# Kernel optimization log

Hardware: AMD Instinct MI355X
Metric: run time of the kernel (lower is better)

The kernel has to match this reference:

```python
import jax, jax.numpy as jnp
import numpy as np

D_MODEL = 1024
NUM_EXP = 64
EPS = 1e-9
B, L = 16, 2048


def setup_inputs() -> dict:
    key = jax.random.key(0)
    ks = jax.random.split(key, 12)
    s = 1.0 / np.sqrt(D_MODEL)
    inp = {
        "x": jax.random.normal(ks[0], (B, L, D_MODEL), dtype=jnp.float32),
        "n_indexes": jax.random.randint(ks[1], (B, NUM_EXP), 0, NUM_EXP),
        "mask": jax.random.randint(ks[2], (B, 1, L), 0, 2).astype(jnp.int32),
        "q_emb": jax.random.normal(ks[3], (NUM_EXP, D_MODEL), dtype=jnp.float32),
        "b_emb": jax.random.normal(ks[4], (NUM_EXP, D_MODEL), dtype=jnp.float32),
        "Wk": jax.random.normal(ks[5], (D_MODEL, D_MODEL), dtype=jnp.float32) * s,
        "bk": jnp.zeros((D_MODEL,), jnp.float32),
        "Wa": jax.random.normal(ks[6], (D_MODEL, D_MODEL), dtype=jnp.float32) * s,
        "ba": jnp.zeros((D_MODEL,), jnp.float32),
        "Wb": jax.random.normal(ks[7], (D_MODEL, D_MODEL), dtype=jnp.float32) * s,
        "bb": jnp.zeros((D_MODEL,), jnp.float32),
        "Ws": jax.random.normal(ks[8], (D_MODEL, D_MODEL), dtype=jnp.float32) * s,
        "bs": jnp.zeros((D_MODEL,), jnp.float32),
    }
    return inp


def reference(x, n_indexes, mask, q_emb, b_emb, Wk, bk, Wa, ba, Wb, bb, Ws, bs):
    # Dropout layers act as identity (eval mode).
    query_exp = q_emb[n_indexes]          # [B, E, D]
    bias_exp = b_emb[n_indexes]           # [B, E, D]
    x_key = x @ Wk.T + bk                 # [B, L, D]
    z = jnp.einsum('bed,bld->bel', query_exp, x_key) / np.sqrt(D_MODEL)  # [B, E, L]

    maskf = (mask != 0).astype(z.dtype)   # broadcast [B,1,L]
    class_a_fw = jax.nn.relu(z) * maskf
    class_b_fw = jax.nn.relu(-z) * maskf
    class_a_fw = class_a_fw / (class_a_fw.sum(-1, keepdims=True) + EPS)
    class_b_fw = class_b_fw / (class_b_fw.sum(-1, keepdims=True) + EPS)

    class_a = jnp.einsum('bel,bld->bed', class_a_fw, x @ Wa.T + ba) + bias_exp
    class_b = jnp.einsum('bel,bld->bed', class_b_fw, x @ Wb.T + bb) + bias_exp

    zt = jnp.swapaxes(z, -2, -1)          # [B, L, E]  (unmasked, as in source)
    class_a_bw = jax.nn.relu(zt)
    class_b_bw = jax.nn.relu(-zt)
    class_a_bw = class_a_bw / (class_a_bw.sum(-1, keepdims=True) + EPS)
    class_b_bw = class_b_bw / (class_b_bw.sum(-1, keepdims=True) + EPS)

    class_a = jnp.einsum('ble,bed->bld', class_a_bw, class_a)  # [B, L, D]
    class_b = jnp.einsum('ble,bed->bld', class_b_bw, class_b)

    selector = jax.nn.sigmoid(x @ Ws.T + bs)
    return selector * class_a + (1.0 - selector) * class_b
```

## Files before the change

### kernel.cpp

```cpp
#include <hip/hip_runtime.h>
#include <math.h>

#define D_MODEL 1024
#define NUM_EXP 64
#define B_SZ 16
#define L_SZ 2048

using bf16x8  = __attribute__((ext_vector_type(8))) __bf16;
using floatx4 = __attribute__((ext_vector_type(4))) float;
using ushort8 = __attribute__((ext_vector_type(8))) unsigned short;
using ushort4v = __attribute__((ext_vector_type(4))) unsigned short;

__device__ __forceinline__ unsigned short f2bf(float f) {
    union { float f; unsigned u; } x; x.f = f;
    unsigned r = (x.u + 0x7fffu + ((x.u >> 16) & 1u)) >> 16;
    return (unsigned short)r;
}
__device__ __forceinline__ float bf2f(unsigned short h) {
    union { unsigned u; float f; } x; x.u = ((unsigned)h) << 16;
    return x.f;
}

#define GLD16(gp, lp) __builtin_amdgcn_global_load_lds( \
    (const __attribute__((address_space(1))) unsigned int*)(gp), \
    (__attribute__((address_space(3))) unsigned int*)(lp), 16, 0, 0)

__global__ void k_convx(const float* __restrict__ in, unsigned short* __restrict__ outN,
                        unsigned short* __restrict__ outT)
{
    __shared__ unsigned short T[64][65];
    const int b = blockIdx.z;
    const int l0 = blockIdx.y * 64, c0 = blockIdx.x * 64;
    const int t = threadIdx.x;
    const int tr = t >> 4, tc = (t & 15) * 4;
    const float* src = in + ((long)b * L_SZ + l0) * D_MODEL + c0;
    unsigned short* dN = outN + ((long)b * L_SZ + l0) * D_MODEL + c0;
    #pragma unroll
    for (int i = 0; i < 4; i++) {
        int r = tr + i * 16;
        float4 v = *(const float4*)(src + (long)r * D_MODEL + tc);
        ushort4v u; u[0]=f2bf(v.x); u[1]=f2bf(v.y); u[2]=f2bf(v.z); u[3]=f2bf(v.w);
        *(ushort4v*)(dN + (long)r * D_MODEL + tc) = u;
        T[r][tc+0]=u[0]; T[r][tc+1]=u[1]; T[r][tc+2]=u[2]; T[r][tc+3]=u[3];
    }
    __syncthreads();
    unsigned short* dT = outT + ((long)b * D_MODEL + c0) * L_SZ + l0;
    #pragma unroll
    for (int i = 0; i < 4; i++) {
        int c = tr + i * 16;
        ushort4v u;
        u[0]=T[tc+0][c]; u[1]=T[tc+1][c]; u[2]=T[tc+2][c]; u[3]=T[tc+3][c];
        *(ushort4v*)(dT + (long)c * L_SZ + tc) = u;
    }
}

__global__ void k_transw(const float* __restrict__ in, unsigned short* __restrict__ outT)
{
    __shared__ unsigned short T[64][65];
    const int r0 = blockIdx.y * 64, c0 = blockIdx.x * 64;
    const int t = threadIdx.x;
    const int tr = t >> 4, tc = (t & 15) * 4;
    const float* src = in + (long)r0 * D_MODEL + c0;
    #pragma unroll
    for (int i = 0; i < 4; i++) {
        int r = tr + i * 16;
        float4 v = *(const float4*)(src + (long)r * D_MODEL + tc);
        T[r][tc+0]=f2bf(v.x); T[r][tc+1]=f2bf(v.y); T[r][tc+2]=f2bf(v.z); T[r][tc+3]=f2bf(v.w);
    }
    __syncthreads();
    unsigned short* dT = outT + ((long)c0) * D_MODEL + r0;
    #pragma unroll
    for (int i = 0; i < 4; i++) {
        int c = tr + i * 16;
        ushort4v u;
        u[0]=T[tc+0][c]; u[1]=T[tc+1][c]; u[2]=T[tc+2][c]; u[3]=T[tc+3][c];
        *(ushort4v*)(dT + (long)c * D_MODEL + tc) = u;
    }
}

__global__ void k_convert3(const float* __restrict__ a, const float* __restrict__ b,
                           const float* __restrict__ c,
                           unsigned short* __restrict__ oa, unsigned short* __restrict__ ob,
                           unsigned short* __restrict__ oc)
{
    long i = ((long)blockIdx.x * 256 + threadIdx.x) * 8;
    int which = (int)(i >> 20);
    long off = i & ((1L << 20) - 1);
    const float* src = which == 0 ? a : which == 1 ? b : c;
    unsigned short* dst = which == 0 ? oa : which == 1 ? ob : oc;
    float4 v0 = *(const float4*)(src + off);
    float4 v1 = *(const float4*)(src + off + 4);
    ushort8 r;
    r[0]=f2bf(v0.x); r[1]=f2bf(v0.y); r[2]=f2bf(v0.z); r[3]=f2bf(v0.w);
    r[4]=f2bf(v1.x); r[5]=f2bf(v1.y); r[6]=f2bf(v1.z); r[7]=f2bf(v1.w);
    *(ushort8*)(dst + off) = r;
}

__global__ void k_gather(const int* __restrict__ idx, const float* __restrict__ q_emb,
                         const float* __restrict__ b_emb, const float* __restrict__ bk,
                         unsigned short* __restrict__ qexp, float* __restrict__ bias_exp,
                         float* __restrict__ qbk)
{
    int be = blockIdx.x;
    int row = idx[be];
    int t = threadIdx.x;
    const float* qs = q_emb + (long)row * D_MODEL;
    const float* bsrc = b_emb + (long)row * D_MODEL;
    float4 q4 = *(const float4*)(qs + t * 4);
    float4 k4 = *(const float4*)(bk + t * 4);
    float4 b4 = *(const float4*)(bsrc + t * 4);
    ushort4v r; r[0]=f2bf(q4.x); r[1]=f2bf(q4.y); r[2]=f2bf(q4.z); r[3]=f2bf(q4.w);
    *(ushort4v*)(qexp + (long)be * D_MODEL + t * 4) = r;
    *(float4*)(bias_exp + (long)be * D_MODEL + t * 4) = b4;
    float p = q4.x*k4.x + q4.y*k4.y + q4.z*k4.z + q4.w*k4.w;
    #pragma unroll
    for (int o = 32; o > 0; o >>= 1) p += __shfl_down(p, o);
    __shared__ float red[4];
    if ((t & 63) == 0) red[t >> 6] = p;
    __syncthreads();
    if (t == 0) qbk[be] = red[0] + red[1] + red[2] + red[3];
}

__launch_bounds__(256)
__global__ void k_gemm_bt(const unsigned short* __restrict__ A,
                          const unsigned short* __restrict__ Bm,
                          const float* __restrict__ rowbias,
                          void* __restrict__ Cout,
                          int M, int N, int K, float scale, int flags,
                          long sA, long sB, long sC)
{
    __shared__ __align__(16) unsigned short As[64 * 32];
    __shared__ __align__(16) unsigned short Bs[64 * 32];
    const int bz = blockIdx.z;
    const unsigned short* Ab = A + (long)bz * sA;
    const unsigned short* Bb = Bm + (long)bz * sB;
    const int tid = threadIdx.x;
    const int wave = tid >> 6, lane = tid & 63;
    const int m0 = blockIdx.y * 64, n0 = blockIdx.x * 64;
    const int lrow = tid >> 2, lk = (tid & 3) * 8;
    const int q = lane >> 4, mr = lane & 15;

    floatx4 acc[4];
    floatx4 z4 = {0.f, 0.f, 0.f, 0.f};
    #pragma unroll
    for (int j = 0; j < 4; j++) acc[j] = z4;

    const unsigned short* Aptr = Ab + (long)(m0 + lrow) * K + lk;
    const unsigned short* Bptr = Bb + (long)(n0 + lrow) * K + lk;

    for (int k0 = 0; k0 < K; k0 += 32) {
        __syncthreads();
        *(ushort8*)&As[lrow * 32 + lk] = *(const ushort8*)(Aptr + k0);
        *(ushort8*)&Bs[lrow * 32 + lk] = *(const ushort8*)(Bptr + k0);
        __syncthreads();
        bf16x8 af = *(const bf16x8*)&As[(wave * 16 + mr) * 32 + q * 8];
        #pragma unroll
        for (int j = 0; j < 4; j++) {
            bf16x8 bfr = *(const bf16x8*)&Bs[(j * 16 + mr) * 32 + q * 8];
            acc[j] = __builtin_amdgcn_mfma_f32_16x16x32_bf16(af, bfr, acc[j], 0, 0, 0);
        }
    }
    #pragma unroll
    for (int j = 0; j < 4; j++) {
        int gn = n0 + j * 16 + mr;
        #pragma unroll
        for (int r = 0; r < 4; r++) {
            int gm = m0 + wave * 16 + q * 4 + r;
            float v = acc[j][r];
            if (rowbias) v += rowbias[(long)bz * M + gm];
            v *= scale;
            long cidx = (long)bz * sC + (long)gm * N + gn;
            if (flags & 1) ((unsigned short*)Cout)[cidx] = f2bf(v);
            else           ((float*)Cout)[cidx] = v;
        }
    }
}

__launch_bounds__(256)
__global__ void k_gemm_fw2(const unsigned short* __restrict__ A1,
                           const unsigned short* __restrict__ A2,
                           const unsigned short* __restrict__ Bt,
                           unsigned short* __restrict__ C1,
                           unsigned short* __restrict__ C2)
{
    __shared__ __align__(16) unsigned short As1[64 * 32];
    __shared__ __align__(16) unsigned short As2[64 * 32];
    __shared__ __align__(16) unsigned short Bs[64 * 32];
    const int bz = blockIdx.z;
    const int n0 = blockIdx.x * 64;
    const int tid = threadIdx.x;
    const int wave = tid >> 6, lane = tid & 63;
    const int lrow = tid >> 2, lk = (tid & 3) * 8;
    const int q = lane >> 4, mr = lane & 15;

    const unsigned short* a1p = A1 + ((long)bz * NUM_EXP + lrow) * L_SZ + lk;
    const unsigned short* a2p = A2 + ((long)bz * NUM_EXP + lrow) * L_SZ + lk;
    const unsigned short* bp  = Bt + ((long)bz * D_MODEL + n0 + lrow) * L_SZ + lk;

    floatx4 acc1[4], acc2[4];
    floatx4 z4 = {0.f, 0.f, 0.f, 0.f};
    #pragma unroll
    for (int j = 0; j < 4; j++) { acc1[j] = z4; acc2[j] = z4; }

    for (int k0 = 0; k0 < L_SZ; k0 += 32) {
        __syncthreads();
        *(ushort8*)&As1[lrow * 32 + lk] = *(const ushort8*)(a1p + k0);
        *(ushort8*)&As2[lrow * 32 + lk] = *(const ushort8*)(a2p + k0);
        *(ushort8*)&Bs[lrow * 32 + lk]  = *(const ushort8*)(bp + k0);
        __syncthreads();
        bf16x8 f1 = *(const bf16x8*)&As1[(wave * 16 + mr) * 32 + q * 8];
        bf16x8 f2 = *(const bf16x8*)&As2[(wave * 16 + mr) * 32 + q * 8];
        #pragma unroll
        for (int j = 0; j < 4; j++) {
            bf16x8 bb = *(const bf16x8*)&Bs[(j * 16 + mr) * 32 + q * 8];
            acc1[j] = __builtin_amdgcn_mfma_f32_16x16x32_bf16(f1, bb, acc1[j], 0, 0, 0);
            acc2[j] = __builtin_amdgcn_mfma_f32_16x16x32_bf16(f2, bb, acc2[j], 0, 0, 0);
        }
    }
    #pragma unroll
    for (int j = 0; j < 4; j++) {
        int gn = n0 + j * 16 + mr;
        #pragma unroll
        for (int r = 0; r < 4; r++) {
            int gm = wave * 16 + q * 4 + r;
            long cidx = ((long)bz * NUM_EXP + gm) * D_MODEL + gn;
            C1[cidx] = f2bf(acc1[j][r]);
            C2[cidx] = f2bf(acc2[j][r]);
        }
    }
}

__launch_bounds__(256)
__global__ void k_gemm_cls(const unsigned short* __restrict__ fwxA, const unsigned short* __restrict__ fwxB,
                           const unsigned short* __restrict__ Wa_, const unsigned short* __restrict__ Wb_,
                           const float* __restrict__ ba_, const float* __restrict__ bb_,
                           const float* __restrict__ wsA, const float* __restrict__ wsB,
                           const float* __restrict__ biasE,
                           unsigned short* __restrict__ aHi, unsigned short* __restrict__ aLo,
                           unsigned short* __restrict__ bHi, unsigned short* __restrict__ bLo)
{
    __shared__ __align__(16) unsigned short As[64 * 32];
    __shared__ __align__(16) unsigned short Bs[64 * 32];
    const int zz = blockIdx.z;
    const int side = zz >> 4, bz = zz & 15;
    const unsigned short* Ab = (side ? fwxB : fwxA) + (long)bz * NUM_EXP * D_MODEL;
    const unsigned short* Bb = side ? Wb_ : Wa_;
    const float* cb = side ? bb_ : ba_;
    const float* rw = (side ? wsB : wsA) + bz * NUM_EXP;
    const float* bE = biasE + (long)bz * NUM_EXP * D_MODEL;
    unsigned short* oHi = (side ? bHi : aHi) + (long)bz * NUM_EXP * D_MODEL;
    unsigned short* oLo = (side ? bLo : aLo) + (long)bz * NUM_EXP * D_MODEL;

    const int tid = threadIdx.x;
    const int wave = tid >> 6, lane = tid & 63;
    const int n0 = blockIdx.x * 64;
    const int lrow = tid >> 2, lk = (tid & 3) * 8;
    const int q = lane >> 4, mr = lane & 15;

    floatx4 acc[4];
    floatx4 z4 = {0.f, 0.f, 0.f, 0.f};
    #pragma unroll
    for (int j = 0; j < 4; j++) acc[j] = z4;

    const unsigned short* Aptr = Ab + (long)lrow * D_MODEL + lk;
    const unsigned short* Bptr = Bb + (long)(n0 + lrow) * D_MODEL + lk;

    for (int k0 = 0; k0 < D_MODEL; k0 += 32) {
        __syncthreads();
        *(ushort8*)&As[lrow * 32 + lk] = *(const ushort8*)(Aptr + k0);
        *(ushort8*)&Bs[lrow * 32 + lk] = *(const ushort8*)(Bptr + k0);
        __syncthreads();
        bf16x8 af = *(const bf16x8*)&As[(wave * 16 + mr) * 32 + q * 8];
        #pragma unroll
        for (int j = 0; j < 4; j++) {
            bf16x8 bfr = *(const bf16x8*)&Bs[(j * 16 + mr) * 32 + q * 8];
            acc[j] = __builtin_amdgcn_mfma_f32_16x16x32_bf16(af, bfr, acc[j], 0, 0, 0);
        }
    }
    #pragma unroll
    for (int j = 0; j < 4; j++) {
        int gn = n0 + j * 16 + mr;
        float cbv = cb[gn];
        #pragma unroll
        for (int r = 0; r < 4; r++) {
            int gm = wave * 16 + q * 4 + r;
            float v = acc[j][r] + rw[gm] * cbv + bE[(long)gm * D_MODEL + gn];
            unsigned short hi = f2bf(v);
            long tix = (long)gn * NUM_EXP + gm;
            oHi[tix] = hi;
            oLo[tix] = f2bf(v - bf2f(hi));
        }
    }
}

__launch_bounds__(256)
__global__ void k_gemm_sel(const unsigned short* __restrict__ A,
                           const unsigned short* __restrict__ Bm,
                           const float* __restrict__ bias,
                           unsigned short* __restrict__ C)
{
    __shared__ __align__(16) unsigned short As[128 * 32];
    __shared__ __align__(16) unsigned short Bs[128 * 32];
    const int tid = threadIdx.x;
    const int wave = tid >> 6, lane = tid & 63;
    const int q = lane >> 4, mr = lane & 15;
    const int wm = wave & 1, wn = wave >> 1;
    const int blk = blockIdx.x;
    const int m0 = ((blk & 7) * 32 + (blk >> 6)) * 128;
    const int n0 = ((blk >> 3) & 7) * 128;

    int rows[2], kofs8[2];
    #pragma unroll
    for (int c = 0; c < 2; c++) {
        int s = c * 256 + tid;
        int row = s >> 2;
        rows[c] = row;
        kofs8[c] = ((s & 3) ^ ((row >> 1) & 3)) * 8;
    }
    const unsigned short* gA0 = A + (long)(m0 + rows[0]) * 1024 + kofs8[0];
    const unsigned short* gA1 = A + (long)(m0 + rows[1]) * 1024 + kofs8[1];
    const unsigned short* gB0 = Bm + (long)(n0 + rows[0]) * 1024 + kofs8[0];
    const unsigned short* gB1 = Bm + (long)(n0 + rows[1]) * 1024 + kofs8[1];
    unsigned short* LA0 = &As[(0 * 256 + wave * 64) * 8];
    unsigned short* LA1 = &As[(1 * 256 + wave * 64) * 8];
    unsigned short* LB0 = &Bs[(0 * 256 + wave * 64) * 8];
    unsigned short* LB1 = &Bs[(1 * 256 + wave * 64) * 8];

    floatx4 acc[4][4];
    floatx4 z4 = {0.f, 0.f, 0.f, 0.f};
    #pragma unroll
    for (int i = 0; i < 4; i++)
        #pragma unroll
        for (int j = 0; j < 4; j++) acc[i][j] = z4;

    const int kread = (q ^ ((mr >> 1) & 3)) * 8;

    for (int k0 = 0; k0 < 1024; k0 += 32) {
        __syncthreads();
        GLD16(gA0 + k0, LA0);
        GLD16(gA1 + k0, LA1);
        GLD16(gB0 + k0, LB0);
        GLD16(gB1 + k0, LB1);
        __syncthreads();
        bf16x8 af[4], bfv[4];
        #pragma unroll
        for (int i = 0; i < 4; i++)
            af[i] = *(const bf16x8*)&As[(wm * 64 + i * 16 + mr) * 32 + kread];
        #pragma unroll
        for (int j = 0; j < 4; j++)
            bfv[j] = *(const bf16x8*)&Bs[(wn * 64 + j * 16 + mr) * 32 + kread];
        #pragma unroll
        for (int i = 0; i < 4; i++)
            #pragma unroll
            for (int j = 0; j < 4; j++)
                acc[i][j] = __builtin_amdgcn_mfma_f32_16x16x32_bf16(af[i], bfv[j], acc[i][j], 0, 0, 0);
    }

    #pragma unroll
    for (int i = 0; i < 4; i++) {
        #pragma unroll
        for (int j = 0; j < 4; j++) {
            int gn = n0 + wn * 64 + j * 16 + mr;
            float cbv = bias[gn];
            #pragma unroll
            for (int r = 0; r < 4; r++) {
                int gm = m0 + wm * 64 + i * 16 + q * 4 + r;
                C[(long)gm * 1024 + gn] = f2bf(acc[i][j][r] + cbv);
            }
        }
    }
}

__global__ void k_fwnorm(const float* __restrict__ z, const int* __restrict__ mask,
                         unsigned short* __restrict__ a_fw, unsigned short* __restrict__ b_fw,
                         float* __restrict__ wsum_a, float* __restrict__ wsum_b)
{
    int be = blockIdx.x;
    int b = be >> 6;
    const float* zr = z + (long)be * L_SZ;
    const int* mr = mask + (long)b * L_SZ;
    int tid = threadIdx.x;
    float sa = 0.f, sb = 0.f;
    for (int l = tid; l < L_SZ; l += 256) {
        float v = zr[l];
        if (mr[l] != 0) { sa += fmaxf(v, 0.f); sb += fmaxf(-v, 0.f); }
    }
    #pragma unroll
    for (int o = 32; o > 0; o >>= 1) { sa += __shfl_down(sa, o); sb += __shfl_down(sb, o); }
    __shared__ float red[8];
    int wave = tid >> 6, lane = tid & 63;
    if (lane == 0) { red[wave] = sa; red[4 + wave] = sb; }
    __syncthreads();
    float ta = red[0] + red[1] + red[2] + red[3];
    float tb = red[4] + red[5] + red[6] + red[7];
    float ia = 1.f / (ta + 1e-9f), ib = 1.f / (tb + 1e-9f);
    if (tid == 0) { wsum_a[be] = ta * ia; wsum_b[be] = tb * ib; }
    for (int l = tid; l < L_SZ; l += 256) {
        float v = zr[l];
        float m = (mr[l] != 0) ? 1.f : 0.f;
        a_fw[(long)be * L_SZ + l] = f2bf(fmaxf(v, 0.f) * m * ia);
        b_fw[(long)be * L_SZ + l] = f2bf(fmaxf(-v, 0.f) * m * ib);
    }
}

__global__ void k_bwnorm(const float* __restrict__ z, unsigned short* __restrict__ a_bw,
                         unsigned short* __restrict__ b_bw)
{
    int r = blockIdx.x * 256 + threadIdx.x;
    int b = r >> 11, l = r & 2047;
    const float* zb = z + (long)b * NUM_EXP * L_SZ + l;
    float sa = 0.f, sb = 0.f;
    float va[NUM_EXP];
    #pragma unroll 8
    for (int e = 0; e < NUM_EXP; e++) {
        float v = zb[(long)e * L_SZ];
        va[e] = v;
        sa += fmaxf(v, 0.f); sb += fmaxf(-v, 0.f);
    }
    float ia = 1.f / (sa + 1e-9f), ib = 1.f / (sb + 1e-9f);
    unsigned short* ar = a_bw + (long)r * NUM_EXP;
    unsigned short* br = b_bw + (long)r * NUM_EXP;
    #pragma unroll 8
    for (int e = 0; e < NUM_EXP; e++) {
        float v = va[e];
        ar[e] = f2bf(fmaxf(v, 0.f) * ia);
        br[e] = f2bf(fmaxf(-v, 0.f) * ib);
    }
}

__launch_bounds__(256)
__global__ void k_final_mfma(const unsigned short* __restrict__ aw,
                             const unsigned short* __restrict__ bw,
                             const unsigned short* __restrict__ caHi,
                             const unsigned short* __restrict__ caLo,
                             const unsigned short* __restrict__ cbHi,
                             const unsigned short* __restrict__ cbLo,
                             const unsigned short* __restrict__ selbf,
                             float* __restrict__ out)
{
    __shared__ __align__(16) unsigned short Aa[64 * 72];
    __shared__ __align__(16) unsigned short Ab[64 * 72];
    __shared__ __align__(16) unsigned short BaH[64 * 72];
    __shared__ __align__(16) unsigned short BaL[64 * 72];
    __shared__ __align__(16) unsigned short BbH[64 * 72];
    __shared__ __align__(16) unsigned short BbL[64 * 72];
    const int bz = blockIdx.z;
    const int l0 = blockIdx.y * 64, d0 = blockIdx.x * 64;
    const int tid = threadIdx.x;
    const int wave = tid >> 6, lane = tid & 63;
    const int q = lane >> 4, mr = lane & 15;

    const unsigned short* awb = aw + ((long)bz * L_SZ + l0) * NUM_EXP;
    const unsigned short* bwb = bw + ((long)bz * L_SZ + l0) * NUM_EXP;
    const long cbase = ((long)bz * D_MODEL + d0) * NUM_EXP;

    #pragma unroll
    for (int c = 0; c < 2; c++) {
        int idx = c * 256 + tid;
        int row = idx >> 3, kc = (idx & 7) * 8;
        int lw = row * 72 + kc;
        long ga = (long)row * NUM_EXP + kc;
        *(ushort8*)&Aa[lw]  = *(const ushort8*)(awb + ga);
        *(ushort8*)&Ab[lw]  = *(const ushort8*)(bwb + ga);
        *(ushort8*)&BaH[lw] = *(const ushort8*)(caHi + cbase + ga);
        *(ushort8*)&BaL[lw] = *(const ushort8*)(caLo + cbase + ga);
        *(ushort8*)&BbH[lw] = *(const ushort8*)(cbHi + cbase + ga);
        *(ushort8*)&BbL[lw] = *(const ushort8*)(cbLo + cbase + ga);
    }
    __syncthreads();

    floatx4 accA[4], accB[4];
    floatx4 z4 = {0.f, 0.f, 0.f, 0.f};
    #pragma unroll
    for (int j = 0; j < 4; j++) { accA[j] = z4; accB[j] = z4; }

    #pragma unroll
    for (int ks = 0; ks < 2; ks++) {
        int ko = ks * 32 + q * 8;
        bf16x8 fa = *(const bf16x8*)&Aa[(wave * 16 + mr) * 72 + ko];
        bf16x8 fb = *(const bf16x8*)&Ab[(wave * 16 + mr) * 72 + ko];
        #pragma unroll
        for (int j = 0; j < 4; j++) {
            int bo = (j * 16 + mr) * 72 + ko;
            accA[j] = __builtin_amdgcn_mfma_f32_16x16x32_bf16(fa, *(const bf16x8*)&BaH[bo], accA[j], 0, 0, 0);
            accA[j] = __builtin_amdgcn_mfma_f32_16x16x32_bf16(fa, *(const bf16x8*)&BaL[bo], accA[j], 0, 0, 0);
            accB[j] = __builtin_amdgcn_mfma_f32_16x16x32_bf16(fb, *(const bf16x8*)&BbH[bo], accB[j], 0, 0, 0);
            accB[j] = __builtin_amdgcn_mfma_f32_16x16x32_bf16(fb, *(const bf16x8*)&BbL[bo], accB[j], 0, 0, 0);
        }
    }

    #pragma unroll
    for (int j = 0; j < 4; j++) {
        #pragma unroll
        for (int r = 0; r < 4; r++) {
            int gl = l0 + wave * 16 + q * 4 + r;
            int gd = d0 + j * 16 + mr;
            long o = ((long)bz * L_SZ + gl) * D_MODEL + gd;
            float s = 1.f / (1.f + __expf(-bf2f(selbf[o])));
            out[o] = s * accA[j][r] + (1.f - s) * accB[j][r];
        }
    }
}

extern "C" void kernel_launch(void* const* d_in, const int* in_sizes, int n_in,
                              void* d_out, int out_size, void* d_ws, size_t ws_size,
                              hipStream_t stream)
{
    const float* x     = (const float*)d_in[0];
    const int*   nidx  = (const int*)d_in[1];
    const int*   mask  = (const int*)d_in[2];
    const float* q_emb = (const float*)d_in[3];
    const float* b_emb = (const float*)d_in[4];
    const float* Wk    = (const float*)d_in[5];
    const float* bk    = (const float*)d_in[6];
    const float* Wa    = (const float*)d_in[7];
    const float* ba    = (const float*)d_in[8];
    const float* Wb    = (const float*)d_in[9];
    const float* bb    = (const float*)d_in[10];
    const float* Ws    = (const float*)d_in[11];
    const float* bs    = (const float*)d_in[12];
    float* out = (float*)d_out;

    constexpr long BLD = (long)B_SZ * L_SZ * D_MODEL;
    constexpr long BEL = (long)B_SZ * NUM_EXP * L_SZ;
    constexpr long BED = (long)B_SZ * NUM_EXP * D_MODEL;
    constexpr long DD  = (long)D_MODEL * D_MODEL;

    char* w = (char*)d_ws;
    size_t off = 0;
    auto carve = [&](size_t bytes) { char* p = w + off; off += (bytes + 255) & ~(size_t)255; return p; };
    unsigned short* x_bf   = (unsigned short*)carve(BLD * 2);
    unsigned short* x_bfT  = (unsigned short*)carve(BLD * 2);
    unsigned short* wkT_bf = (unsigned short*)carve(DD * 2);
    unsigned short* wa_bf  = (unsigned short*)carve(DD * 2);
    unsigned short* wb_bf  = (unsigned short*)carve(DD * 2);
    unsigned short* ws_bf  = (unsigned short*)carve(DD * 2);
    unsigned short* qexp   = (unsigned short*)carve(BED * 2);
    float*          bias_e = (float*)carve(BED * 4);
    float*          qbk    = (float*)carve(B_SZ * NUM_EXP * 4);
    unsigned short* qk     = (unsigned short*)carve(BED * 2);
    float*          z      = (float*)carve(BEL * 4);
    unsigned short* a_fw   = (unsigned short*)carve(BEL * 2);
    unsigned short* b_fw   = (unsigned short*)carve(BEL * 2);
    float*          wsum_a = (float*)carve(B_SZ * NUM_EXP * 4);
    float*          wsum_b = (float*)carve(B_SZ * NUM_EXP * 4);
    unsigned short* a_bw   = (unsigned short*)carve(BEL * 2);
    unsigned short* b_bw   = (unsigned short*)carve(BEL * 2);
    unsigned short* fwx_a  = (unsigned short*)carve(BED * 2);
    unsigned short* fwx_b  = (unsigned short*)carve(BED * 2);
    unsigned short* caHi   = (unsigned short*)carve(BED * 2);
    unsigned short* caLo   = (unsigned short*)carve(BED * 2);
    unsigned short* cbHi   = (unsigned short*)carve(BED * 2);
    unsigned short* cbLo   = (unsigned short*)carve(BED * 2);
    if (ws_size < off) return;
    unsigned short* selbf = x_bfT;

    k_convx<<<dim3(16, 32, B_SZ), 256, 0, stream>>>(x, x_bf, x_bfT);
    k_transw<<<dim3(16, 16), 256, 0, stream>>>(Wk, wkT_bf);
    k_convert3<<<(3 * DD) / 2048, 256, 0, stream>>>(Wa, Wb, Ws, wa_bf, wb_bf, ws_bf);
    k_gather<<<B_SZ * NUM_EXP, 256, 0, stream>>>(nidx, q_emb, b_emb, bk, qexp, bias_e, qbk);

    k_gemm_bt<<<dim3(16, 1, B_SZ), 256, 0, stream>>>(qexp, wkT_bf, nullptr, qk,
        NUM_EXP, D_MODEL, D_MODEL, 1.f, 1, (long)NUM_EXP * D_MODEL, 0, (long)NUM_EXP * D_MODEL);

    k_gemm_bt<<<dim3(32, 1, B_SZ), 256, 0, stream>>>(qk, x_bf, qbk, z,
        NUM_EXP, L_SZ, D_MODEL, 1.f / 32.f, 0,
        (long)NUM_EXP * D_MODEL, (long)L_SZ * D_MODEL, (long)NUM_EXP * L_SZ);

    k_fwnorm<<<B_SZ * NUM_EXP, 256, 0, stream>>>(z, mask, a_fw, b_fw, wsum_a, wsum_b);
    k_bwnorm<<<(B_SZ * L_SZ) / 256, 256, 0, stream>>>(z, a_bw, b_bw);

    k_gemm_fw2<<<dim3(16, 1, B_SZ), 256, 0, stream>>>(a_fw, b_fw, x_bfT, fwx_a, fwx_b);

    k_gemm_sel<<<2048, 256, 0, stream>>>(x_bf, ws_bf, bs, selbf);

    k_gemm_cls<<<dim3(16, 1, 32), 256, 0, stream>>>(fwx_a, fwx_b, wa_bf, wb_bf, ba, bb,
        wsum_a, wsum_b, bias_e, caHi, caLo, cbHi, cbLo);

    k_final_mfma<<<dim3(16, 32, B_SZ), 256, 0, stream>>>(a_bw, b_bw, caHi, caLo, cbHi, cbLo, selbf, out);
}
```

Measured before the change: 546.3 us.

## Rewrite selector GEMM with 256x256 tiles and multi-stage async LDS pipeline

The selector GEMM goes from 128x128 tiles with a synchronous load-then-compute loop to 256x256 tiles on 512-thread blocks. Global loads go straight to LDS with double buffering and stay several stages ahead of compute. The MFMA blocks are interleaved with barriers and priority hints. The aim is to hide memory latency behind MFMA work and raise data reuse per block. In exchange it uses more LDS and registers, and relies on hand-tuned vmcnt waits that must stay correct.

```diff
diff --git a/kernel.cpp b/kernel.cpp
--- a/kernel.cpp
+++ b/kernel.cpp
@@ -293,78 +293,101 @@
     }
 }
 
-__launch_bounds__(256)
+__launch_bounds__(512, 2)
 __global__ void k_gemm_sel(const unsigned short* __restrict__ A,
                            const unsigned short* __restrict__ Bm,
                            const float* __restrict__ bias,
                            unsigned short* __restrict__ C)
 {
-    __shared__ __align__(16) unsigned short As[128 * 32];
-    __shared__ __align__(16) unsigned short Bs[128 * 32];
+    __shared__ __align__(16) unsigned short As[2][2][8192];
+    __shared__ __align__(16) unsigned short Bs[2][2][8192];
+
     const int tid = threadIdx.x;
-    const int wave = tid >> 6, lane = tid & 63;
+    const int wid = tid >> 6, lane = tid & 63;
     const int q = lane >> 4, mr = lane & 15;
-    const int wm = wave & 1, wn = wave >> 1;
-    const int blk = blockIdx.x;
-    const int m0 = ((blk & 7) * 32 + (blk >> 6)) * 128;
-    const int n0 = ((blk >> 3) & 7) * 128;
-
-    int rows[2], kofs8[2];
-    #pragma unroll
-    for (int c = 0; c < 2; c++) {
-        int s = c * 256 + tid;
-        int row = s >> 2;
-        rows[c] = row;
-        kofs8[c] = ((s & 3) ^ ((row >> 1) & 3)) * 8;
-    }
-    const unsigned short* gA0 = A + (long)(m0 + rows[0]) * 1024 + kofs8[0];
-    const unsigned short* gA1 = A + (long)(m0 + rows[1]) * 1024 + kofs8[1];
-    const unsigned short* gB0 = Bm + (long)(n0 + rows[0]) * 1024 + kofs8[0];
-    const unsigned short* gB1 = Bm + (long)(n0 + rows[1]) * 1024 + kofs8[1];
-    unsigned short* LA0 = &As[(0 * 256 + wave * 64) * 8];
-    unsigned short* LA1 = &As[(1 * 256 + wave * 64) * 8];
-    unsigned short* LB0 = &Bs[(0 * 256 + wave * 64) * 8];
-    unsigned short* LB1 = &Bs[(1 * 256 + wave * 64) * 8];
-
-    floatx4 acc[4][4];
+    const int wm = wid >> 2, wn = wid & 3;
+    const int kread = (q ^ ((mr >> 1) & 3)) * 8;
+
+    const int bid = blockIdx.x;
+    const int wg = (bid & 7) * 64 + (bid >> 3);
+    const int m0 = (wg >> 2) * 256;
+    const int n0 = (wg & 3) * 256;
+
+    const unsigned short* Ag = A + (long)m0 * 1024;
+    const unsigned short* Bg = Bm + (long)n0 * 1024;
+
+    const int srow = tid >> 2;
+    const int sgrp = (tid & 3) ^ ((srow >> 1) & 3);
+    const long soff = (long)srow * 1024 + sgrp * 8;
+    const int ldst = wid * 64 * 8;
+
+    auto STAGE = [&](int g) {
+        int tile = g >> 2; if (tile > 15) tile = 15;
+        const int kh = (g >> 1) & 1, isB = g & 1;
+        const unsigned short* src = (isB ? Bg : Ag) + (long)tile * 64 + kh * 32 + soff;
+        unsigned short* dst = (isB ? &Bs[0][0][0] : &As[0][0][0])
+                              + ((tile & 1) * 2 + kh) * 8192 + ldst;
+        GLD16(src, dst);
+        GLD16(src + 128 * 1024, dst + 4096);
+    };
+
+    floatx4 acc[8][4];
     floatx4 z4 = {0.f, 0.f, 0.f, 0.f};
     #pragma unroll
-    for (int i = 0; i < 4; i++)
+    for (int i = 0; i < 8; i++)
         #pragma unroll
         for (int j = 0; j < 4; j++) acc[i][j] = z4;
 
-    const int kread = (q ^ ((mr >> 1) & 3)) * 8;
-
-    for (int k0 = 0; k0 < 1024; k0 += 32) {
-        __syncthreads();
-        GLD16(gA0 + k0, LA0);
-        GLD16(gA1 + k0, LA1);
-        GLD16(gB0 + k0, LB0);
-        GLD16(gB1 + k0, LB1);
-        __syncthreads();
-        bf16x8 af[4], bfv[4];
-        #pragma unroll
-        for (int i = 0; i < 4; i++)
-            af[i] = *(const bf16x8*)&As[(wm * 64 + i * 16 + mr) * 32 + kread];
-        #pragma unroll
-        for (int j = 0; j < 4; j++)
-            bfv[j] = *(const bf16x8*)&Bs[(wn * 64 + j * 16 + mr) * 32 + kread];
-        #pragma unroll
-        for (int i = 0; i < 4; i++)
+    STAGE(0); STAGE(1); STAGE(2); STAGE(3); STAGE(4); STAGE(5);
+    asm volatile("s_waitcnt vmcnt(4)" ::: "memory");
+    __builtin_amdgcn_s_barrier();
+
+    for (int t = 0; t < 16; t++) {
+        const unsigned short* Abuf = &As[t & 1][0][0];
+        const unsigned short* Bbuf = &Bs[t & 1][0][0];
+        bf16x8 bfr[4];
+        #pragma unroll
+        for (int p = 0; p < 4; p++) {
+            const int kh = p >> 1, mh = p & 1;
+            bf16x8 af[4];
             #pragma unroll
-            for (int j = 0; j < 4; j++)
-                acc[i][j] = __builtin_amdgcn_mfma_f32_16x16x32_bf16(af[i], bfv[j], acc[i][j], 0, 0, 0);
-    }
-
-    #pragma unroll
-    for (int i = 0; i < 4; i++) {
+            for (int i = 0; i < 4; i++)
+                af[i] = *(const bf16x8*)&Abuf[kh * 8192 +
+                        (wm * 128 + mh * 64 + i * 16 + mr) * 32 + kread];
+            if (mh == 0) {
+                #pragma unroll
+                for (int j = 0; j < 4; j++)
+                    bfr[j] = *(const bf16x8*)&Bbuf[kh * 8192 +
+                             (wn * 64 + j * 16 + mr) * 32 + kread];
+            }
+            STAGE(4 * t + p + 6);
+            if (mh == 1) asm volatile("s_waitcnt vmcnt(8)" ::: "memory");
+            __builtin_amdgcn_s_barrier();
+            asm volatile("s_waitcnt lgkmcnt(0)" ::: "memory");
+            __builtin_amdgcn_sched_barrier(0);
+            __builtin_amdgcn_s_setprio(1);
+            #pragma unroll
+            for (int i = 0; i < 4; i++)
+                #pragma unroll
+                for (int j = 0; j < 4; j++)
+                    acc[mh * 4 + i][j] = __builtin_amdgcn_mfma_f32_16x16x32_bf16(
+                        af[i], bfr[j], acc[mh * 4 + i][j], 0, 0, 0);
+            __builtin_amdgcn_s_setprio(0);
+            __builtin_amdgcn_s_barrier();
+            __builtin_amdgcn_sched_barrier(0);
+        }
+    }
+    asm volatile("s_waitcnt vmcnt(0)" ::: "memory");
+
+    #pragma unroll
+    for (int i = 0; i < 8; i++) {
         #pragma unroll
         for (int j = 0; j < 4; j++) {
-            int gn = n0 + wn * 64 + j * 16 + mr;
-            float cbv = bias[gn];
+            const int gn = n0 + wn * 64 + j * 16 + mr;
+            const float cbv = bias[gn];
             #pragma unroll
             for (int r = 0; r < 4; r++) {
-                int gm = m0 + wm * 64 + i * 16 + q * 4 + r;
+                const int gm = m0 + wm * 128 + i * 16 + q * 4 + r;
                 C[(long)gm * 1024 + gn] = f2bf(acc[i][j][r] + cbv);
             }
         }
@@ -572,7 +595,7 @@
 
     k_gemm_fw2<<<dim3(16, 1, B_SZ), 256, 0, stream>>>(a_fw, b_fw, x_bfT, fwx_a, fwx_b);
 
-    k_gemm_sel<<<2048, 256, 0, stream>>>(x_bf, ws_bf, bs, selbf);
+    k_gemm_sel<<<512, 512, 0, stream>>>(x_bf, ws_bf, bs, selbf);
 
     k_gemm_cls<<<dim3(16, 1, 32), 256, 0, stream>>>(fwx_a, fwx_b, wa_bf, wb_bf, ba, bb,
         wsum_a, wsum_b, bias_e, caHi, caLo, cbHi, cbLo);
```

Result: no change. 548.4 us (+0.4%).
